# Kernel tuning notes

Hardware: AMD Instinct MI355X
Metric: run time of the kernel (lower is better)

The kernel has to match this reference:

```python
import jax, jax.numpy as jnp
import numpy as np

E = 8        # num_experts
D_IN = 512   # num_inputs
H = 256      # num_neurons_expert
T = 64       # num_neurons_tower
B = 16384    # batch


def setup_inputs() -> dict:
    key = jax.random.key(0)
    ks = jax.random.split(key, 7)
    s_in = 1.0 / np.sqrt(D_IN)
    s_h = 1.0 / np.sqrt(H)
    return {
        "xv": jax.random.normal(ks[0], (B, D_IN), dtype=jnp.float32),
        # expert weights stacked: torch Linear weight is (out,in) -> (E, H, D_IN)
        "We": jax.random.uniform(ks[1], (E, H, D_IN), jnp.float32, -s_in, s_in),
        "be": jax.random.uniform(ks[2], (E, H), jnp.float32, -s_in, s_in),
        "Wg": jax.random.uniform(ks[3], (E, D_IN), jnp.float32, -s_in, s_in),
        "bg": jax.random.uniform(ks[4], (E,), jnp.float32, -s_in, s_in),
        "Wt": jax.random.uniform(ks[5], (T, H), jnp.float32, -s_h, s_h),
        "bt": jax.random.uniform(ks[6], (T,), jnp.float32, -s_h, s_h),
    }


def reference(xv, We, be, Wg, bg, Wt, bt):
    # All experts as one batched GEMM: [B,D] x [E,H,D] -> [B,E,H]
    experts = jax.nn.relu(jnp.einsum("bd,ehd->beh", xv, We) + be[None, :, :])
    # Dropout is identity in eval mode.
    gate = jax.nn.softmax(xv @ Wg.T + bg, axis=1)            # [B,E]
    combined = jnp.einsum("beh,be->bh", experts, gate)        # [B,H]
    out = jax.nn.sigmoid(combined @ Wt.T + bt)                # [B,T]
    return out
```

## Files before the change

### kernel.cpp

```cpp
#include <hip/hip_runtime.h>
#include <stdint.h>

typedef unsigned short u16;
typedef __bf16 bf16x8 __attribute__((ext_vector_type(8)));
typedef float f32x4 __attribute__((ext_vector_type(4)));

#define XV_N 8388608
#define WE_N 1048576
#define WT_N 16384

__device__ __forceinline__ void glds16(const void* g, void* l) {
  __builtin_amdgcn_global_load_lds(
      (const __attribute__((address_space(1))) unsigned int*)g,
      (__attribute__((address_space(3))) unsigned int*)l, 16, 0, 0);
}

__device__ __forceinline__ u16 f2bf(float f) {
  unsigned int u = __builtin_bit_cast(unsigned int, f);
  u += 0x7fffu + ((u >> 16) & 1u);
  return (u16)(u >> 16);
}

__device__ __forceinline__ float bf2f(u16 u) {
  return __builtin_bit_cast(float, ((unsigned int)u) << 16);
}

__global__ __launch_bounds__(256) void convert_kernel(
    const float* __restrict__ xv, const float* __restrict__ We,
    const float* __restrict__ Wt, u16* __restrict__ dst) {
  int idx = (blockIdx.x * 256 + threadIdx.x) * 8;
  const float* src;
  if (idx < XV_N) src = xv + idx;
  else if (idx < XV_N + WE_N) src = We + (idx - XV_N);
  else src = Wt + (idx - XV_N - WE_N);
  float4 a = *(const float4*)src;
  float4 b = *(const float4*)(src + 4);
  uint4 o;
  o.x = (unsigned)f2bf(a.x) | ((unsigned)f2bf(a.y) << 16);
  o.y = (unsigned)f2bf(a.z) | ((unsigned)f2bf(a.w) << 16);
  o.z = (unsigned)f2bf(b.x) | ((unsigned)f2bf(b.y) << 16);
  o.w = (unsigned)f2bf(b.z) | ((unsigned)f2bf(b.w) << 16);
  *(uint4*)(dst + idx) = o;
}

__global__ __launch_bounds__(256) void gate_kernel(
    const u16* __restrict__ xv_bf, const float* __restrict__ Wg,
    const float* __restrict__ bg, float* __restrict__ gate) {
  const int tid = threadIdx.x, wid = tid >> 6, lane = tid & 63;
  const int rsub = lane >> 3, ksub = lane & 7;
  const int row = blockIdx.x * 32 + wid * 8 + rsub;
  const u16* xr = xv_bf + row * 512 + ksub * 64;
  float s[8] = {0.f, 0.f, 0.f, 0.f, 0.f, 0.f, 0.f, 0.f};
#pragma unroll
  for (int j = 0; j < 8; j++) {
    uint4 xp = *(const uint4*)(xr + j * 8);
    float x[8];
    x[0] = bf2f((u16)xp.x); x[1] = bf2f((u16)(xp.x >> 16));
    x[2] = bf2f((u16)xp.y); x[3] = bf2f((u16)(xp.y >> 16));
    x[4] = bf2f((u16)xp.z); x[5] = bf2f((u16)(xp.z >> 16));
    x[6] = bf2f((u16)xp.w); x[7] = bf2f((u16)(xp.w >> 16));
#pragma unroll
    for (int e = 0; e < 8; e++) {
      const float* wg = Wg + e * 512 + ksub * 64 + j * 8;
      float4 w0 = *(const float4*)wg;
      float4 w1 = *(const float4*)(wg + 4);
      s[e] += x[0] * w0.x + x[1] * w0.y + x[2] * w0.z + x[3] * w0.w +
              x[4] * w1.x + x[5] * w1.y + x[6] * w1.z + x[7] * w1.w;
    }
  }
#pragma unroll
  for (int e = 0; e < 8; e++) {
    s[e] += __shfl_xor(s[e], 1);
    s[e] += __shfl_xor(s[e], 2);
    s[e] += __shfl_xor(s[e], 4);
    s[e] += bg[e];
  }
  float mx = s[0];
#pragma unroll
  for (int e = 1; e < 8; e++) mx = fmaxf(mx, s[e]);
  float p[8], sum = 0.f;
#pragma unroll
  for (int e = 0; e < 8; e++) { p[e] = __expf(s[e] - mx); sum += p[e]; }
  float inv = 1.f / sum;
  if (ksub == 0) {
    float4 g0 = {p[0] * inv, p[1] * inv, p[2] * inv, p[3] * inv};
    float4 g1 = {p[4] * inv, p[5] * inv, p[6] * inv, p[7] * inv};
    *(float4*)(gate + row * 8) = g0;
    *(float4*)(gate + row * 8 + 4) = g1;
  }
}

__global__ __launch_bounds__(512, 2) void moe_main(
    const u16* __restrict__ xv_bf, const u16* __restrict__ We_bf,
    const float* __restrict__ be, const float* __restrict__ gate,
    const u16* __restrict__ Wt_bf, u16* __restrict__ part) {
  __shared__ u16 lds[24576];

  const int bx = blockIdx.x;
  const int mb = bx & 127, sub = bx >> 7;
  const int ep = sub >> 1, hb = sub & 1;
  const int m0 = mb << 7, h0 = hb << 7, eg0 = ep << 2;
  const int tid = threadIdx.x, lane = tid & 63, wid = tid >> 6;
  const int wm = wid >> 2, wn = wid & 3;
  const int l15 = lane & 15, l4 = lane >> 4;

  f32x4 acc[4][4][2];
#pragma unroll
  for (int e = 0; e < 4; e++)
#pragma unroll
    for (int mt = 0; mt < 4; mt++)
#pragma unroll
      for (int nt = 0; nt < 2; nt++) acc[e][mt][nt] = {0.f, 0.f, 0.f, 0.f};

  for (int kc = 0; kc < 8; kc++) {
    const int kofs = kc << 6;
    __syncthreads();
#pragma unroll
    for (int r = 0; r < 2; r++) {
      int gi = r * 512 + tid;
      int row = gi >> 3, s = gi & 7, g = s ^ (row & 7);
      glds16(xv_bf + ((m0 + row) << 9) + kofs + (g << 3), &lds[gi << 3]);
    }
#pragma unroll
    for (int r = 0; r < 4; r++) {
      int gi = r * 512 + tid;
      int el = gi >> 10, rem = gi & 1023, n = rem >> 3, s = rem & 7, g = s ^ (n & 7);
      glds16(We_bf + ((eg0 + el) << 17) + ((h0 + n) << 9) + kofs + (g << 3),
             &lds[8192 + (gi << 3)]);
    }
    __syncthreads();
    bf16x8 af[4][2];
#pragma unroll
    for (int mt = 0; mt < 4; mt++)
#pragma unroll
      for (int ks = 0; ks < 2; ks++) {
        int row = wm * 64 + mt * 16 + l15;
        int gg = ks * 4 + l4;
        int slot = gg ^ (row & 7);
        af[mt][ks] = *(const bf16x8*)&lds[(row << 6) + (slot << 3)];
      }
#pragma unroll
    for (int el = 0; el < 2; el++)
#pragma unroll
      for (int ks = 0; ks < 2; ks++) {
        bf16x8 bf[2];
#pragma unroll
        for (int nt = 0; nt < 2; nt++) {
          int n = wn * 32 + nt * 16 + l15;
          int gg = ks * 4 + l4;
          int slot = gg ^ (n & 7);
          bf[nt] = *(const bf16x8*)&lds[8192 + (el << 13) + (n << 6) + (slot << 3)];
        }
#pragma unroll
        for (int mt = 0; mt < 4; mt++)
#pragma unroll
          for (int nt = 0; nt < 2; nt++)
            acc[el][mt][nt] = __builtin_amdgcn_mfma_f32_16x16x32_bf16(
                af[mt][ks], bf[nt], acc[el][mt][nt], 0, 0, 0);
      }
    __syncthreads();
#pragma unroll
    for (int r = 0; r < 4; r++) {
      int gi = r * 512 + tid;
      int el = gi >> 10, rem = gi & 1023, n = rem >> 3, s = rem & 7, g = s ^ (n & 7);
      glds16(We_bf + ((eg0 + 2 + el) << 17) + ((h0 + n) << 9) + kofs + (g << 3),
             &lds[8192 + (gi << 3)]);
    }
    __syncthreads();
#pragma unroll
    for (int el = 0; el < 2; el++)
#pragma unroll
      for (int ks = 0; ks < 2; ks++) {
        bf16x8 bf[2];
#pragma unroll
        for (int nt = 0; nt < 2; nt++) {
          int n = wn * 32 + nt * 16 + l15;
          int gg = ks * 4 + l4;
          int slot = gg ^ (n & 7);
          bf[nt] = *(const bf16x8*)&lds[8192 + (el << 13) + (n << 6) + (slot << 3)];
        }
#pragma unroll
        for (int mt = 0; mt < 4; mt++)
#pragma unroll
          for (int nt = 0; nt < 2; nt++)
            acc[2 + el][mt][nt] = __builtin_amdgcn_mfma_f32_16x16x32_bf16(
                af[mt][ks], bf[nt], acc[2 + el][mt][nt], 0, 0, 0);
      }
  }

  float bev[4][2];
#pragma unroll
  for (int e = 0; e < 4; e++)
#pragma unroll
    for (int nt = 0; nt < 2; nt++)
      bev[e][nt] = be[(eg0 + e) * 256 + h0 + wn * 32 + nt * 16 + l15];

  f32x4 comb[4][2];
#pragma unroll
  for (int mt = 0; mt < 4; mt++) {
#pragma unroll
    for (int i = 0; i < 4; i++) {
      int row = m0 + wm * 64 + mt * 16 + l4 * 4 + i;
      float4 gv4 = *(const float4*)&gate[(row << 3) + eg0];
      const float* gv = &gv4.x;
#pragma unroll
      for (int nt = 0; nt < 2; nt++) {
        float c = 0.f;
#pragma unroll
        for (int e = 0; e < 4; e++)
          c += gv[e] * fmaxf(acc[e][mt][nt][i] + bev[e][nt], 0.f);
        comb[mt][nt][i] = c;
      }
    }
  }

  __syncthreads();
#pragma unroll
  for (int mt = 0; mt < 4; mt++)
#pragma unroll
    for (int i = 0; i < 4; i++) {
      int row = wm * 64 + mt * 16 + l4 * 4 + i;
#pragma unroll
      for (int nt = 0; nt < 2; nt++) {
        int col = wn * 32 + nt * 16 + l15;
        lds[row * 136 + col] = f2bf(comb[mt][nt][i]);
      }
    }
  __syncthreads();
  f32x4 tacc[4];
#pragma unroll
  for (int nt = 0; nt < 4; nt++) tacc[nt] = {0.f, 0.f, 0.f, 0.f};
  const int trow = wid * 16 + l15;
#pragma unroll
  for (int ks = 0; ks < 4; ks++) {
    bf16x8 aT = *(const bf16x8*)&lds[trow * 136 + ks * 32 + l4 * 8];
#pragma unroll
    for (int nt = 0; nt < 4; nt++) {
      bf16x8 bT = *(const bf16x8*)&Wt_bf[(nt * 16 + l15) * 256 + h0 + ks * 32 + l4 * 8];
      tacc[nt] = __builtin_amdgcn_mfma_f32_16x16x32_bf16(aT, bT, tacc[nt], 0, 0, 0);
    }
  }
  u16* pout = part + sub * 1048576;
#pragma unroll
  for (int nt = 0; nt < 4; nt++)
#pragma unroll
    for (int i = 0; i < 4; i++) {
      int grow = m0 + wid * 16 + l4 * 4 + i;
      pout[grow * 64 + nt * 16 + l15] = f2bf(tacc[nt][i]);
    }
}

__global__ __launch_bounds__(256) void finish_kernel(
    const u16* __restrict__ part, const float* __restrict__ bt,
    float* __restrict__ out) {
  const int base = (blockIdx.x * 256 + threadIdx.x) * 8;
  float a[8] = {0.f, 0.f, 0.f, 0.f, 0.f, 0.f, 0.f, 0.f};
#pragma unroll
  for (int s = 0; s < 4; s++) {
    uint4 p = *(const uint4*)(part + s * 1048576 + base);
    a[0] += bf2f((u16)p.x); a[1] += bf2f((u16)(p.x >> 16));
    a[2] += bf2f((u16)p.y); a[3] += bf2f((u16)(p.y >> 16));
    a[4] += bf2f((u16)p.z); a[5] += bf2f((u16)(p.z >> 16));
    a[6] += bf2f((u16)p.w); a[7] += bf2f((u16)(p.w >> 16));
  }
  const int t0 = base & 63;
  float4 b0 = *(const float4*)(bt + t0);
  float4 b1 = *(const float4*)(bt + t0 + 4);
  const float* bb = &b0.x;
  float r[8];
#pragma unroll
  for (int j = 0; j < 8; j++) {
    float bj = (j < 4) ? bb[j] : (&b1.x)[j - 4];
    r[j] = 1.f / (1.f + __expf(-(a[j] + bj)));
  }
  float4 o0 = {r[0], r[1], r[2], r[3]};
  float4 o1 = {r[4], r[5], r[6], r[7]};
  *(float4*)(out + base) = o0;
  *(float4*)(out + base + 4) = o1;
}

extern "C" void kernel_launch(void* const* d_in, const int* in_sizes, int n_in,
                              void* d_out, int out_size, void* d_ws, size_t ws_size,
                              hipStream_t stream) {
  const float* xv = (const float*)d_in[0];
  const float* We = (const float*)d_in[1];
  const float* be = (const float*)d_in[2];
  const float* Wg = (const float*)d_in[3];
  const float* bg = (const float*)d_in[4];
  const float* Wt = (const float*)d_in[5];
  const float* bt = (const float*)d_in[6];

  char* ws = (char*)d_ws;
  u16* cvt = (u16*)ws;
  u16* xv_bf = cvt;
  u16* We_bf = cvt + XV_N;
  u16* Wt_bf = cvt + XV_N + WE_N;
  float* gate = (float*)(ws + 18907136);
  u16* part = (u16*)(ws + 19431424);

  convert_kernel<<<4616, 256, 0, stream>>>(xv, We, Wt, cvt);
  gate_kernel<<<512, 256, 0, stream>>>(xv_bf, Wg, bg, gate);
  moe_main<<<512, 512, 0, stream>>>(xv_bf, We_bf, be, gate, Wt_bf, part);
  finish_kernel<<<512, 256, 0, stream>>>(part, bt, (float*)d_out);
}
```

Baseline: 178.5 us.

## Fuse conversion, gating, MoE GEMM and finish into one kernel

Drops the separate fp32-to-bf16 conversion, gate and finish kernels and folds everything into a single kernel. Inputs are read as fp32 and converted while being staged into LDS, and the gate logits are computed with MFMA on the same x tiles. The last block for each row tile, found with an atomic counter, reduces the four partial outputs and applies the sigmoid. This removes the bf16 copy of x round-tripping through memory and several launches. In exchange, x is loaded as fp32 (twice the bytes) by each of the 4 sub-blocks, the synchronous loads replace the async LDS loads, and the larger LDS footprint may lower occupancy.

```diff
diff --git a/kernel.cpp b/kernel.cpp
--- a/kernel.cpp
+++ b/kernel.cpp
@@ -5,96 +5,35 @@
 typedef __bf16 bf16x8 __attribute__((ext_vector_type(8)));
 typedef float f32x4 __attribute__((ext_vector_type(4)));
 
-#define XV_N 8388608
-#define WE_N 1048576
-#define WT_N 16384
-
-__device__ __forceinline__ void glds16(const void* g, void* l) {
-  __builtin_amdgcn_global_load_lds(
-      (const __attribute__((address_space(1))) unsigned int*)g,
-      (__attribute__((address_space(3))) unsigned int*)l, 16, 0, 0);
-}
+#define GATE_OFF 20480
 
 __device__ __forceinline__ u16 f2bf(float f) {
   unsigned int u = __builtin_bit_cast(unsigned int, f);
   u += 0x7fffu + ((u >> 16) & 1u);
   return (u16)(u >> 16);
 }
-
+__device__ __forceinline__ unsigned pk2(float lo, float hi) {
+  return (unsigned)f2bf(lo) | ((unsigned)f2bf(hi) << 16);
+}
+__device__ __forceinline__ uint4 cvt8(float4 a, float4 b) {
+  uint4 o;
+  o.x = pk2(a.x, a.y);
+  o.y = pk2(a.z, a.w);
+  o.z = pk2(b.x, b.y);
+  o.w = pk2(b.z, b.w);
+  return o;
+}
 __device__ __forceinline__ float bf2f(u16 u) {
-  return __builtin_bit_cast(float, ((unsigned int)u) << 16);
-}
-
-__global__ __launch_bounds__(256) void convert_kernel(
+  return __builtin_bit_cast(float, ((unsigned)u) << 16);
+}
+
+__global__ __launch_bounds__(512, 2) void moe_fused(
     const float* __restrict__ xv, const float* __restrict__ We,
-    const float* __restrict__ Wt, u16* __restrict__ dst) {
-  int idx = (blockIdx.x * 256 + threadIdx.x) * 8;
-  const float* src;
-  if (idx < XV_N) src = xv + idx;
-  else if (idx < XV_N + WE_N) src = We + (idx - XV_N);
-  else src = Wt + (idx - XV_N - WE_N);
-  float4 a = *(const float4*)src;
-  float4 b = *(const float4*)(src + 4);
-  uint4 o;
-  o.x = (unsigned)f2bf(a.x) | ((unsigned)f2bf(a.y) << 16);
-  o.y = (unsigned)f2bf(a.z) | ((unsigned)f2bf(a.w) << 16);
-  o.z = (unsigned)f2bf(b.x) | ((unsigned)f2bf(b.y) << 16);
-  o.w = (unsigned)f2bf(b.z) | ((unsigned)f2bf(b.w) << 16);
-  *(uint4*)(dst + idx) = o;
-}
-
-__global__ __launch_bounds__(256) void gate_kernel(
-    const u16* __restrict__ xv_bf, const float* __restrict__ Wg,
-    const float* __restrict__ bg, float* __restrict__ gate) {
-  const int tid = threadIdx.x, wid = tid >> 6, lane = tid & 63;
-  const int rsub = lane >> 3, ksub = lane & 7;
-  const int row = blockIdx.x * 32 + wid * 8 + rsub;
-  const u16* xr = xv_bf + row * 512 + ksub * 64;
-  float s[8] = {0.f, 0.f, 0.f, 0.f, 0.f, 0.f, 0.f, 0.f};
-#pragma unroll
-  for (int j = 0; j < 8; j++) {
-    uint4 xp = *(const uint4*)(xr + j * 8);
-    float x[8];
-    x[0] = bf2f((u16)xp.x); x[1] = bf2f((u16)(xp.x >> 16));
-    x[2] = bf2f((u16)xp.y); x[3] = bf2f((u16)(xp.y >> 16));
-    x[4] = bf2f((u16)xp.z); x[5] = bf2f((u16)(xp.z >> 16));
-    x[6] = bf2f((u16)xp.w); x[7] = bf2f((u16)(xp.w >> 16));
-#pragma unroll
-    for (int e = 0; e < 8; e++) {
-      const float* wg = Wg + e * 512 + ksub * 64 + j * 8;
-      float4 w0 = *(const float4*)wg;
-      float4 w1 = *(const float4*)(wg + 4);
-      s[e] += x[0] * w0.x + x[1] * w0.y + x[2] * w0.z + x[3] * w0.w +
-              x[4] * w1.x + x[5] * w1.y + x[6] * w1.z + x[7] * w1.w;
-    }
-  }
-#pragma unroll
-  for (int e = 0; e < 8; e++) {
-    s[e] += __shfl_xor(s[e], 1);
-    s[e] += __shfl_xor(s[e], 2);
-    s[e] += __shfl_xor(s[e], 4);
-    s[e] += bg[e];
-  }
-  float mx = s[0];
-#pragma unroll
-  for (int e = 1; e < 8; e++) mx = fmaxf(mx, s[e]);
-  float p[8], sum = 0.f;
-#pragma unroll
-  for (int e = 0; e < 8; e++) { p[e] = __expf(s[e] - mx); sum += p[e]; }
-  float inv = 1.f / sum;
-  if (ksub == 0) {
-    float4 g0 = {p[0] * inv, p[1] * inv, p[2] * inv, p[3] * inv};
-    float4 g1 = {p[4] * inv, p[5] * inv, p[6] * inv, p[7] * inv};
-    *(float4*)(gate + row * 8) = g0;
-    *(float4*)(gate + row * 8 + 4) = g1;
-  }
-}
-
-__global__ __launch_bounds__(512, 2) void moe_main(
-    const u16* __restrict__ xv_bf, const u16* __restrict__ We_bf,
-    const float* __restrict__ be, const float* __restrict__ gate,
-    const u16* __restrict__ Wt_bf, u16* __restrict__ part) {
-  __shared__ u16 lds[24576];
+    const float* __restrict__ be, const float* __restrict__ Wg,
+    const float* __restrict__ bg, const float* __restrict__ Wt,
+    const float* __restrict__ bt, u16* __restrict__ part,
+    unsigned* __restrict__ counters, float* __restrict__ out) {
+  __shared__ u16 lds[40960];
 
   const int bx = blockIdx.x;
   const int mb = bx & 127, sub = bx >> 7;
@@ -111,22 +50,42 @@
     for (int mt = 0; mt < 4; mt++)
 #pragma unroll
       for (int nt = 0; nt < 2; nt++) acc[e][mt][nt] = {0.f, 0.f, 0.f, 0.f};
+  f32x4 gacc[4];
+#pragma unroll
+  for (int mt = 0; mt < 4; mt++) gacc[mt] = {0.f, 0.f, 0.f, 0.f};
 
   for (int kc = 0; kc < 8; kc++) {
     const int kofs = kc << 6;
     __syncthreads();
 #pragma unroll
+    for (int r = 0; r < 8; r++) {
+      int gbi = r * 512 + tid;
+      int el = gbi >> 10, rem = gbi & 1023, n = rem >> 3, g = rem & 7;
+      const float* src = We + ((eg0 + el) << 17) + ((h0 + n) << 9) + kofs + (g << 3);
+      float4 a = *(const float4*)src;
+      float4 b = *(const float4*)(src + 4);
+      int slot = g ^ (n & 7);
+      *(uint4*)&lds[8192 + (el << 13) + (n << 6) + (slot << 3)] = cvt8(a, b);
+    }
+#pragma unroll
     for (int r = 0; r < 2; r++) {
-      int gi = r * 512 + tid;
-      int row = gi >> 3, s = gi & 7, g = s ^ (row & 7);
-      glds16(xv_bf + ((m0 + row) << 9) + kofs + (g << 3), &lds[gi << 3]);
-    }
-#pragma unroll
-    for (int r = 0; r < 4; r++) {
-      int gi = r * 512 + tid;
-      int el = gi >> 10, rem = gi & 1023, n = rem >> 3, s = rem & 7, g = s ^ (n & 7);
-      glds16(We_bf + ((eg0 + el) << 17) + ((h0 + n) << 9) + kofs + (g << 3),
-             &lds[8192 + (gi << 3)]);
+      int agi = r * 512 + tid;
+      int m = agi >> 3, g = agi & 7;
+      const float* src = xv + (((m0 + m) << 9) + kofs + (g << 3));
+      float4 a = *(const float4*)src;
+      float4 b = *(const float4*)(src + 4);
+      int slot = g ^ (m & 7);
+      *(uint4*)&lds[(m << 6) + (slot << 3)] = cvt8(a, b);
+    }
+    bf16x8 wgf[2];
+    if (wn == 0) {
+#pragma unroll
+      for (int ks = 0; ks < 2; ks++) {
+        const float* src = Wg + ((l15 & 7) << 9) + kofs + ks * 32 + (l4 << 3);
+        float4 a = *(const float4*)src;
+        float4 b = *(const float4*)(src + 4);
+        wgf[ks] = __builtin_bit_cast(bf16x8, cvt8(a, b));
+      }
     }
     __syncthreads();
     bf16x8 af[4][2];
@@ -139,54 +98,59 @@
         int slot = gg ^ (row & 7);
         af[mt][ks] = *(const bf16x8*)&lds[(row << 6) + (slot << 3)];
       }
-#pragma unroll
-    for (int el = 0; el < 2; el++)
+    if (wn == 0) {
+#pragma unroll
+      for (int ks = 0; ks < 2; ks++)
+#pragma unroll
+        for (int mt = 0; mt < 4; mt++)
+          gacc[mt] = __builtin_amdgcn_mfma_f32_16x16x32_bf16(
+              af[mt][ks], wgf[ks], gacc[mt], 0, 0, 0);
+    }
+#pragma unroll
+    for (int el = 0; el < 4; el++)
 #pragma unroll
       for (int ks = 0; ks < 2; ks++) {
-        bf16x8 bf[2];
+        bf16x8 bfr[2];
 #pragma unroll
         for (int nt = 0; nt < 2; nt++) {
           int n = wn * 32 + nt * 16 + l15;
           int gg = ks * 4 + l4;
           int slot = gg ^ (n & 7);
-          bf[nt] = *(const bf16x8*)&lds[8192 + (el << 13) + (n << 6) + (slot << 3)];
+          bfr[nt] = *(const bf16x8*)&lds[8192 + (el << 13) + (n << 6) + (slot << 3)];
         }
 #pragma unroll
         for (int mt = 0; mt < 4; mt++)
 #pragma unroll
           for (int nt = 0; nt < 2; nt++)
             acc[el][mt][nt] = __builtin_amdgcn_mfma_f32_16x16x32_bf16(
-                af[mt][ks], bf[nt], acc[el][mt][nt], 0, 0, 0);
-      }
-    __syncthreads();
-#pragma unroll
-    for (int r = 0; r < 4; r++) {
-      int gi = r * 512 + tid;
-      int el = gi >> 10, rem = gi & 1023, n = rem >> 3, s = rem & 7, g = s ^ (n & 7);
-      glds16(We_bf + ((eg0 + 2 + el) << 17) + ((h0 + n) << 9) + kofs + (g << 3),
-             &lds[8192 + (gi << 3)]);
-    }
-    __syncthreads();
-#pragma unroll
-    for (int el = 0; el < 2; el++)
-#pragma unroll
-      for (int ks = 0; ks < 2; ks++) {
-        bf16x8 bf[2];
-#pragma unroll
-        for (int nt = 0; nt < 2; nt++) {
-          int n = wn * 32 + nt * 16 + l15;
-          int gg = ks * 4 + l4;
-          int slot = gg ^ (n & 7);
-          bf[nt] = *(const bf16x8*)&lds[8192 + (el << 13) + (n << 6) + (slot << 3)];
+                af[mt][ks], bfr[nt], acc[el][mt][nt], 0, 0, 0);
+      }
+  }
+
+  __syncthreads();
+  float* gateL = (float*)&lds[GATE_OFF];
+  if (wn == 0) {
+    float bgv = bg[l15 & 7];
+#pragma unroll
+    for (int mt = 0; mt < 4; mt++) {
+#pragma unroll
+      for (int i = 0; i < 4; i++) {
+        float v = gacc[mt][i] + bgv;
+        float mx = fmaxf(v, __shfl_xor(v, 1));
+        mx = fmaxf(mx, __shfl_xor(mx, 2));
+        mx = fmaxf(mx, __shfl_xor(mx, 4));
+        float p = __expf(v - mx);
+        float s = p + __shfl_xor(p, 1);
+        s += __shfl_xor(s, 2);
+        s += __shfl_xor(s, 4);
+        if (l15 < 8) {
+          int row = wm * 64 + mt * 16 + l4 * 4 + i;
+          gateL[row * 8 + l15] = p / s;
         }
-#pragma unroll
-        for (int mt = 0; mt < 4; mt++)
-#pragma unroll
-          for (int nt = 0; nt < 2; nt++)
-            acc[2 + el][mt][nt] = __builtin_amdgcn_mfma_f32_16x16x32_bf16(
-                af[mt][ks], bf[nt], acc[2 + el][mt][nt], 0, 0, 0);
-      }
-  }
+      }
+    }
+  }
+  __syncthreads();
 
   float bev[4][2];
 #pragma unroll
@@ -195,88 +159,85 @@
     for (int nt = 0; nt < 2; nt++)
       bev[e][nt] = be[(eg0 + e) * 256 + h0 + wn * 32 + nt * 16 + l15];
 
-  f32x4 comb[4][2];
 #pragma unroll
   for (int mt = 0; mt < 4; mt++) {
 #pragma unroll
     for (int i = 0; i < 4; i++) {
-      int row = m0 + wm * 64 + mt * 16 + l4 * 4 + i;
-      float4 gv4 = *(const float4*)&gate[(row << 3) + eg0];
-      const float* gv = &gv4.x;
+      int row = wm * 64 + mt * 16 + l4 * 4 + i;
+      float4 g4 = *(const float4*)&gateL[row * 8 + eg0];
+      const float* gv = &g4.x;
 #pragma unroll
       for (int nt = 0; nt < 2; nt++) {
         float c = 0.f;
 #pragma unroll
         for (int e = 0; e < 4; e++)
           c += gv[e] * fmaxf(acc[e][mt][nt][i] + bev[e][nt], 0.f);
-        comb[mt][nt][i] = c;
-      }
-    }
-  }
-
-  __syncthreads();
-#pragma unroll
-  for (int mt = 0; mt < 4; mt++)
+        lds[row * 136 + wn * 32 + nt * 16 + l15] = f2bf(c);
+      }
+    }
+  }
+  __syncthreads();
+
+  f32x4 tacc[4];
+#pragma unroll
+  for (int ntt = 0; ntt < 4; ntt++) tacc[ntt] = {0.f, 0.f, 0.f, 0.f};
+  const int trow = wid * 16 + l15;
+#pragma unroll
+  for (int ks = 0; ks < 4; ks++) {
+    bf16x8 aT = *(const bf16x8*)&lds[trow * 136 + ks * 32 + (l4 << 3)];
+#pragma unroll
+    for (int ntt = 0; ntt < 4; ntt++) {
+      const float* wsrc = Wt + (ntt * 16 + l15) * 256 + h0 + ks * 32 + (l4 << 3);
+      float4 a = *(const float4*)wsrc;
+      float4 b = *(const float4*)(wsrc + 4);
+      bf16x8 bT = __builtin_bit_cast(bf16x8, cvt8(a, b));
+      tacc[ntt] = __builtin_amdgcn_mfma_f32_16x16x32_bf16(aT, bT, tacc[ntt], 0, 0, 0);
+    }
+  }
+  u16* pout = part + (((mb << 2) + sub) << 13);
+#pragma unroll
+  for (int ntt = 0; ntt < 4; ntt++)
 #pragma unroll
     for (int i = 0; i < 4; i++) {
-      int row = wm * 64 + mt * 16 + l4 * 4 + i;
-#pragma unroll
-      for (int nt = 0; nt < 2; nt++) {
-        int col = wn * 32 + nt * 16 + l15;
-        lds[row * 136 + col] = f2bf(comb[mt][nt][i]);
-      }
-    }
-  __syncthreads();
-  f32x4 tacc[4];
-#pragma unroll
-  for (int nt = 0; nt < 4; nt++) tacc[nt] = {0.f, 0.f, 0.f, 0.f};
-  const int trow = wid * 16 + l15;
-#pragma unroll
-  for (int ks = 0; ks < 4; ks++) {
-    bf16x8 aT = *(const bf16x8*)&lds[trow * 136 + ks * 32 + l4 * 8];
-#pragma unroll
-    for (int nt = 0; nt < 4; nt++) {
-      bf16x8 bT = *(const bf16x8*)&Wt_bf[(nt * 16 + l15) * 256 + h0 + ks * 32 + l4 * 8];
-      tacc[nt] = __builtin_amdgcn_mfma_f32_16x16x32_bf16(aT, bT, tacc[nt], 0, 0, 0);
-    }
-  }
-  u16* pout = part + sub * 1048576;
-#pragma unroll
-  for (int nt = 0; nt < 4; nt++)
-#pragma unroll
-    for (int i = 0; i < 4; i++) {
-      int grow = m0 + wid * 16 + l4 * 4 + i;
-      pout[grow * 64 + nt * 16 + l15] = f2bf(tacc[nt][i]);
-    }
-}
-
-__global__ __launch_bounds__(256) void finish_kernel(
-    const u16* __restrict__ part, const float* __restrict__ bt,
-    float* __restrict__ out) {
-  const int base = (blockIdx.x * 256 + threadIdx.x) * 8;
-  float a[8] = {0.f, 0.f, 0.f, 0.f, 0.f, 0.f, 0.f, 0.f};
-#pragma unroll
-  for (int s = 0; s < 4; s++) {
-    uint4 p = *(const uint4*)(part + s * 1048576 + base);
-    a[0] += bf2f((u16)p.x); a[1] += bf2f((u16)(p.x >> 16));
-    a[2] += bf2f((u16)p.y); a[3] += bf2f((u16)(p.y >> 16));
-    a[4] += bf2f((u16)p.z); a[5] += bf2f((u16)(p.z >> 16));
-    a[6] += bf2f((u16)p.w); a[7] += bf2f((u16)(p.w >> 16));
-  }
-  const int t0 = base & 63;
-  float4 b0 = *(const float4*)(bt + t0);
-  float4 b1 = *(const float4*)(bt + t0 + 4);
-  const float* bb = &b0.x;
-  float r[8];
-#pragma unroll
-  for (int j = 0; j < 8; j++) {
-    float bj = (j < 4) ? bb[j] : (&b1.x)[j - 4];
-    r[j] = 1.f / (1.f + __expf(-(a[j] + bj)));
-  }
-  float4 o0 = {r[0], r[1], r[2], r[3]};
-  float4 o1 = {r[4], r[5], r[6], r[7]};
-  *(float4*)(out + base) = o0;
-  *(float4*)(out + base + 4) = o1;
+      int grow = wid * 16 + l4 * 4 + i;
+      pout[grow * 64 + ntt * 16 + l15] = f2bf(tacc[ntt][i]);
+    }
+
+  __threadfence();
+  __syncthreads();
+  unsigned* flag = (unsigned*)&lds[18432];
+  if (tid == 0) *flag = atomicAdd(&counters[mb], 1u);
+  __syncthreads();
+  if (*flag == 3u) {
+    __threadfence();
+    const u16* pbase = part + ((size_t)mb << 15);
+    const int ebase = tid * 16;
+    const int row = ebase >> 6, col0 = ebase & 63;
+    float a[16];
+#pragma unroll
+    for (int j = 0; j < 16; j++) a[j] = 0.f;
+#pragma unroll
+    for (int s = 0; s < 4; s++) {
+      const u16* ps = pbase + s * 8192 + ebase;
+      uint4 p0 = *(const uint4*)ps;
+      uint4 p1 = *(const uint4*)(ps + 8);
+      unsigned w[8] = {p0.x, p0.y, p0.z, p0.w, p1.x, p1.y, p1.z, p1.w};
+#pragma unroll
+      for (int j = 0; j < 8; j++) {
+        a[2 * j] += bf2f((u16)w[j]);
+        a[2 * j + 1] += bf2f((u16)(w[j] >> 16));
+      }
+    }
+#pragma unroll
+    for (int j = 0; j < 16; j++) {
+      float x = a[j] + bt[col0 + j];
+      a[j] = 1.f / (1.f + __expf(-x));
+    }
+    float* dst = out + (m0 + row) * 64 + col0;
+#pragma unroll
+    for (int j = 0; j < 4; j++)
+      *(float4*)(dst + 4 * j) = make_float4(a[4 * j], a[4 * j + 1], a[4 * j + 2], a[4 * j + 3]);
+  }
 }
 
 extern "C" void kernel_launch(void* const* d_in, const int* in_sizes, int n_in,
@@ -291,15 +252,10 @@
   const float* bt = (const float*)d_in[6];
 
   char* ws = (char*)d_ws;
-  u16* cvt = (u16*)ws;
-  u16* xv_bf = cvt;
-  u16* We_bf = cvt + XV_N;
-  u16* Wt_bf = cvt + XV_N + WE_N;
-  float* gate = (float*)(ws + 18907136);
-  u16* part = (u16*)(ws + 19431424);
-
-  convert_kernel<<<4616, 256, 0, stream>>>(xv, We, Wt, cvt);
-  gate_kernel<<<512, 256, 0, stream>>>(xv_bf, Wg, bg, gate);
-  moe_main<<<512, 512, 0, stream>>>(xv_bf, We_bf, be, gate, Wt_bf, part);
-  finish_kernel<<<512, 256, 0, stream>>>(part, bt, (float*)d_out);
-}
+  unsigned* counters = (unsigned*)ws;
+  u16* part = (u16*)(ws + 1024);
+
+  (void)hipMemsetAsync(counters, 0, 512, stream);
+  moe_fused<<<512, 512, 0, stream>>>(xv, We, be, Wg, bg, Wt, bt, part, counters,
+                                     (float*)d_out);
+}
```

New measurement: 332.9 us. 1.86x slower.
